# Optimization experiments

Measured on AMD Instinct MI355X. Metric: run time of the kernel, lower is better.

Reference implementation:

```python
import jax, jax.numpy as jnp
import numpy as np

N = 50000       # nodes
E = 1_600_000   # edges (avg degree 32)
IN = 256        # in_dim
HID = 64        # hidden_dim
HEADS = 2
CLS = 10
NEG_SLOPE = 0.2  # PyG GATConv default leaky_relu slope


def gat_layer(x, edge_index, W, att_src, att_dst, bias, heads, concat):
    """PyG-style GATConv (eval mode, add_self_loops=True).
    x: [N, F_in]; W: [F_in, heads*C]; att_src/att_dst: [heads, C]; bias: [heads*C] or [C].
    """
    n = x.shape[0]
    loop = jnp.arange(n)
    src = jnp.concatenate([edge_index[0], loop])   # message sources j
    dst = jnp.concatenate([edge_index[1], loop])   # message targets i
    C = W.shape[1] // heads
    h = (x @ W).reshape(n, heads, C)               # [N, H, C]
    a_s = jnp.sum(h * att_src, axis=-1)            # [N, H]
    a_d = jnp.sum(h * att_dst, axis=-1)            # [N, H]
    e = jax.nn.leaky_relu(a_s[src] + a_d[dst], NEG_SLOPE)   # [E', H]
    # segment softmax over incoming edges of each destination node
    m = jax.lax.stop_gradient(jax.ops.segment_max(e, dst, num_segments=n))
    ex = jnp.exp(e - m[dst])
    denom = jax.ops.segment_sum(ex, dst, num_segments=n)
    alpha = ex / denom[dst]                         # [E', H]
    out = jax.ops.segment_sum(alpha[:, :, None] * h[src], dst, num_segments=n)  # [N, H, C]
    out = out.reshape(n, heads * C) if concat else out.mean(axis=1)
    return out + bias


def setup_inputs() -> dict:
    key = jax.random.key(0)
    ks = jax.random.split(key, 12)
    sd = lambda f: np.float32(1.0 / np.sqrt(f))
    x = jax.random.normal(ks[0], (N, IN), dtype=jnp.float32)
    edge_index = jax.random.randint(ks[1], (2, E), 0, N, dtype=jnp.int64)
    # layer 1: in_dim -> hidden, heads=2, concat
    W1 = jax.random.normal(ks[2], (IN, HEADS * HID), dtype=jnp.float32) * sd(IN)
    as1 = jax.random.normal(ks[3], (HEADS, HID), dtype=jnp.float32) * sd(HID)
    ad1 = jax.random.normal(ks[4], (HEADS, HID), dtype=jnp.float32) * sd(HID)
    b1 = jnp.zeros((HEADS * HID,), dtype=jnp.float32)
    # layer 2: hidden*heads -> hidden, heads=1, concat=False
    W2 = jax.random.normal(ks[5], (HEADS * HID, HID), dtype=jnp.float32) * sd(HEADS * HID)
    as2 = jax.random.normal(ks[6], (1, HID), dtype=jnp.float32) * sd(HID)
    ad2 = jax.random.normal(ks[7], (1, HID), dtype=jnp.float32) * sd(HID)
    b2 = jnp.zeros((HID,), dtype=jnp.float32)
    # linear head
    Wl = jax.random.normal(ks[8], (HID, CLS), dtype=jnp.float32) * sd(HID)
    bl = jnp.zeros((CLS,), dtype=jnp.float32)
    return {"x": x, "edge_index": edge_index,
            "W1": W1, "as1": as1, "ad1": ad1, "b1": b1,
            "W2": W2, "as2": as2, "ad2": ad2, "b2": b2,
            "Wl": Wl, "bl": bl}


def reference(x, edge_index, W1, as1, ad1, b1, W2, as2, ad2, b2, Wl, bl):
    h = jax.nn.elu(gat_layer(x, edge_index, W1, as1, ad1, b1, HEADS, True))
    h = jax.nn.elu(gat_layer(h, edge_index, W2, as2, ad2, b2, 1, False))
    return h @ Wl + bl  # [N, num_classes]
```

## Files before the change

### kernel.cpp

```cpp
#include <hip/hip_runtime.h>

#define NN 50000
#define NE 1600000
#define EP (NE + NN)
#define IN_DIM 256
#define HIDD 64
#define NCLS 10
#define NBKT 196
#define EPB 8192
#define NPB ((EP + EPB - 1) / EPB)
#define BCAP 12288

typedef unsigned short u16;
typedef short bf16x8 __attribute__((ext_vector_type(8)));
typedef float f32x4 __attribute__((ext_vector_type(4)));
typedef unsigned u32x4 __attribute__((ext_vector_type(4)));

__device__ __forceinline__ float b2f(u16 v) { return __uint_as_float(((unsigned)v) << 16); }
__device__ __forceinline__ u16 f2b(float f) {
    unsigned u = __float_as_uint(f);
    unsigned r = (u + 0x7FFFu + ((u >> 16) & 1u)) >> 16;
    return (u16)r;
}

__device__ __forceinline__ void load_edge(const int* __restrict__ ei, int m, int g,
                                          int& s, int& d) {
    if (g < NE) {
        if (m) { s = ei[2 * (size_t)g]; d = ei[2 * ((size_t)NE + g)]; }
        else   { s = ei[g];             d = ei[NE + g]; }
    } else {
        s = d = g - NE;
    }
    s = s < 0 ? 0 : (s >= NN ? NN - 1 : s);
    d = d < 0 ? 0 : (d >= NN ? NN - 1 : d);
}

__device__ __forceinline__ void wcvt_att_job(
    const float* __restrict__ W, const float* __restrict__ as,
    const float* __restrict__ ad, int K, int N, int H, u16* __restrict__ Wt,
    int idx) {
    if (idx >= K * (N + 16)) return;
    int n = idx / K, k = idx - n * K;
    if (n < N) { Wt[idx] = f2b(W[(size_t)k * N + n]); return; }
    int j = n - N;
    if (j >= 2 * H) { Wt[idx] = 0; return; }
    const float* att = (j & 1) ? ad : as;
    int h = j >> 1, C = N / H;
    float sum = 0.f;
    for (int c = 0; c < C; ++c)
        sum += W[(size_t)k * N + h * C + c] * att[h * C + c];
    Wt[idx] = f2b(sum);
}

__global__ __launch_bounds__(1024) void partition_k(
    const int* __restrict__ ei, int* __restrict__ gcursor,
    unsigned* __restrict__ bbuf,
    const float* __restrict__ W1, const float* __restrict__ as1,
    const float* __restrict__ ad1, u16* __restrict__ w1t,
    const float* __restrict__ W2, const float* __restrict__ as2,
    const float* __restrict__ ad2, u16* __restrict__ w2t) {
    __shared__ int hist[NBKT], base[NBKT], cur[NBKT];
    __shared__ unsigned stash[EPB];
    __shared__ int smode;
    int t = threadIdx.x, b = blockIdx.x;
    if (b < 36) wcvt_att_job(W1, as1, ad1, 256, 128, 2, w1t, b * 1024 + t);
    else if (b < 46) wcvt_att_job(W2, as2, ad2, 128, 64, 1, w2t, (b - 36) * 1024 + t);
    if (t < 64) {
        int nz = 0;
#pragma unroll
        for (int k = 0; k < 4; ++k)
            if (ei[2 * (t * 4 + k) + 1] != 0) nz = 1;
        unsigned long long bal = __ballot(nz);
        if (t == 0) smode = (bal == 0ULL) ? 1 : 0;
    }
    for (int i = t; i < NBKT; i += 1024) hist[i] = 0;
    __syncthreads();
    int m = smode;
    int g0 = b * EPB;
    int gend = min(g0 + EPB, EP);
    for (int g = g0 + t; g < gend; g += 1024) {
        int s, d;
        load_edge(ei, m, g, s, d);
        stash[g - g0] = ((unsigned)s << 16) | (unsigned)d;
        atomicAdd(&hist[d >> 8], 1);
    }
    __syncthreads();
    for (int i = t; i < NBKT; i += 1024) {
        base[i] = hist[i] ? atomicAdd(&gcursor[i], hist[i]) : 0;
        cur[i] = 0;
    }
    __syncthreads();
    int cnt = gend - g0;
    for (int l = t; l < cnt; l += 1024) {
        unsigned p = stash[l];
        int d = p & 0xFFFF;
        int bb = d >> 8;
        int r = base[bb] + atomicAdd(&cur[bb], 1);
        if (r < BCAP)
            bbuf[(size_t)bb * BCAP + r] = ((p >> 16) << 8) | (unsigned)(d & 255);
    }
}

__global__ __launch_bounds__(1024) void bucket_csr_k(const unsigned* __restrict__ bbuf,
                                                     const int* __restrict__ gcursor,
                                                     int* __restrict__ row_ptr,
                                                     u16* __restrict__ csr_src) {
    __shared__ int bsc[256];
    __shared__ int hist[256], scn[256], cur[256];
    __shared__ int se0, scnt, stot;
    int b = blockIdx.x, t = threadIdx.x;
    int v = 0;
    if (t < 256) {
        v = (t < NBKT) ? min(gcursor[t], BCAP) : 0;
        bsc[t] = v;
        hist[t] = 0;
    }
    __syncthreads();
    for (int off = 1; off < 256; off <<= 1) {
        int x = (t < 256 && t >= off) ? bsc[t - off] : 0;
        __syncthreads();
        if (t < 256) bsc[t] += x;
        __syncthreads();
    }
    if (t == b) { se0 = bsc[t] - v; scnt = v; }
    if (t == NBKT - 1) stot = bsc[t];
    __syncthreads();
    int e0 = se0, cnt = scnt;
    const unsigned* bb = bbuf + (size_t)b * BCAP;
    for (int e = t; e < cnt; e += 1024)
        atomicAdd(&hist[bb[e] & 255], 1);
    __syncthreads();
    int hv = 0;
    if (t < 256) { hv = hist[t]; scn[t] = hv; }
    __syncthreads();
    for (int off = 1; off < 256; off <<= 1) {
        int x = (t < 256 && t >= off) ? scn[t - off] : 0;
        __syncthreads();
        if (t < 256) scn[t] += x;
        __syncthreads();
    }
    if (t < 256) {
        int ex = scn[t] - hv;
        int n = b * 256 + t;
        if (n < NN) row_ptr[n] = e0 + ex;
        cur[t] = e0 + ex;
    }
    __syncthreads();
    for (int e = t; e < cnt; e += 1024) {
        unsigned p = bb[e];
        int pos = atomicAdd(&cur[p & 255], 1);
        csr_src[pos] = (u16)(p >> 8);
    }
    if (b == 0 && t == 0) row_ptr[NN] = stot;
}

template <int K, int NF, int H, bool F32A>
__global__ __launch_bounds__(256) void gemm_mfma_att_k(
    const float* __restrict__ Af, const u16* __restrict__ Ab,
    const u16* __restrict__ Wt, u16* __restrict__ C,
    float* __restrict__ a_s, float* __restrict__ a_d) {
    constexpr int NTF = NF / 16, NT = NTF + 1, KS = K / 32;
    const int wave = threadIdx.x >> 6, lane = threadIdx.x & 63;
    const int quad = lane >> 4, l15 = lane & 15;
    const int m0 = blockIdx.x * 64 + wave * 16;
    int rowA = m0 + l15;
    if (rowA >= NN) rowA = NN - 1;
    const float* afp = F32A ? (Af + (size_t)rowA * K + quad * 8) : nullptr;
    const u16*   abp = F32A ? nullptr : (Ab + (size_t)rowA * K + quad * 8);
    const u16* bptr = Wt + (size_t)l15 * K + quad * 8;
    f32x4 acc[NT] = {};
#pragma unroll
    for (int ks = 0; ks < KS; ++ks) {
        bf16x8 af;
        if (F32A) {
            float4 v0 = *(const float4*)(afp + ks * 32);
            float4 v1 = *(const float4*)(afp + ks * 32 + 4);
            af[0] = (short)f2b(v0.x); af[1] = (short)f2b(v0.y);
            af[2] = (short)f2b(v0.z); af[3] = (short)f2b(v0.w);
            af[4] = (short)f2b(v1.x); af[5] = (short)f2b(v1.y);
            af[6] = (short)f2b(v1.z); af[7] = (short)f2b(v1.w);
        } else {
            af = *(const bf16x8*)(abp + ks * 32);
        }
        bf16x8 bf[NT];
#pragma unroll
        for (int nt = 0; nt < NT; ++nt)
            bf[nt] = *(const bf16x8*)(bptr + (size_t)nt * 16 * K + ks * 32);
#pragma unroll
        for (int nt = 0; nt < NT; ++nt)
            acc[nt] = __builtin_amdgcn_mfma_f32_16x16x32_bf16(af, bf[nt], acc[nt], 0, 0, 0);
    }
#pragma unroll
    for (int nt = 0; nt < NTF; ++nt) {
#pragma unroll
        for (int reg = 0; reg < 4; ++reg) {
            int row = m0 + quad * 4 + reg;
            if (row < NN) C[(size_t)row * NF + nt * 16 + l15] = f2b(acc[nt][reg]);
        }
    }
    if (l15 < 2 * H) {
        int h = l15 >> 1;
        float* dst = (l15 & 1) ? a_d : a_s;
#pragma unroll
        for (int reg = 0; reg < 4; ++reg) {
            int row = m0 + quad * 4 + reg;
            if (row < NN) dst[row * H + h] = acc[NTF][reg];
        }
    }
}

template <int CH, int H, bool HEAD>
__global__ __launch_bounds__(256) void gat_gather_k(
    const int* __restrict__ row_ptr, const u16* __restrict__ csr_src,
    const float* __restrict__ att_s, const float* __restrict__ a_d,
    const u16* __restrict__ h, const float* __restrict__ bias,
    u16* __restrict__ outg, const float* __restrict__ Wl,
    const float* __restrict__ bl, float* __restrict__ outh) {
    constexpr int LPR = CH / 8;
    constexpr int G = 64 / LPR;
    constexpr int SH = (CH == 128) ? 8 : 7;
    int n = (blockIdx.x * blockDim.x + threadIdx.x) >> 6;
    int lane = threadIdx.x & 63;
    if (n >= NN) return;
    int r0 = row_ptr[n], r1 = row_ptr[n + 1];
    const int q = lane & (LPR - 1);
    const int g = lane >> ((CH == 128) ? 4 : 3);
    const unsigned qoff = (unsigned)q * 16u;
    const unsigned char* h8 = (const unsigned char*)h;

    float4 av0 = *(const float4*)(att_s + q * 8);
    float4 av1 = *(const float4*)(att_s + q * 8 + 4);
    float attv[8] = {av0.x, av0.y, av0.z, av0.w, av1.x, av1.y, av1.z, av1.w};

    float adn = (H == 2) ? a_d[n * 2 + (q >> 3)] : a_d[n];

    float dh = 0.f;
    float acc[8];
#pragma unroll
    for (int v = 0; v < 8; ++v) acc[v] = 0.f;

    for (int base = r0; base < r1; base += 64) {
        int cnt = min(64, r1 - base);
        int idx = base + lane;
        bool act = idx < r1;
        int slv = act ? ((int)csr_src[idx] | 0x10000) : 0;
        for (int j0 = 0; j0 < cnt; j0 += 4 * G) {
            int sr[4];
#pragma unroll
            for (int i = 0; i < 4; ++i)
                sr[i] = __builtin_amdgcn_ds_bpermute((j0 + i * G + g) << 2, slv);
            u32x4 hv[4];
#pragma unroll
            for (int i = 0; i < 4; ++i)
                hv[i] = *(const u32x4*)(
                    h8 + (((unsigned)(sr[i] & 0xFFFF) << SH) + qoff));
#pragma unroll
            for (int i = 0; i < 4; ++i) {
                float f[8];
#pragma unroll
                for (int k = 0; k < 4; ++k) {
                    unsigned w = hv[i][k];
                    f[2 * k]     = __uint_as_float(w << 16);
                    f[2 * k + 1] = __uint_as_float(w & 0xFFFF0000u);
                }
                float d = f[0] * attv[0];
#pragma unroll
                for (int k = 1; k < 8; ++k) d += f[k] * attv[k];
                d += __shfl_xor(d, 1);
                d += __shfl_xor(d, 2);
                d += __shfl_xor(d, 4);
                float e = d + adn;
                e = e > 0.f ? e : 0.2f * e;
                e = fminf(e, 60.f);
                float ex = __expf(e);
                ex = (sr[i] & 0x10000) ? ex : 0.f;
                dh += ex;
#pragma unroll
                for (int k = 0; k < 8; ++k) acc[k] += ex * f[k];
            }
        }
    }

#pragma unroll
    for (int off = LPR; off < 64; off <<= 1) dh += __shfl_xor(dh, off);
#pragma unroll
    for (int v = 0; v < 8; ++v) {
#pragma unroll
        for (int off = LPR; off < 64; off <<= 1)
            acc[v] += __shfl_xor(acc[v], off);
    }

    if (HEAD) {
        float t01 = (lane & 8) ? acc[1] : acc[0];
        float t23 = (lane & 8) ? acc[3] : acc[2];
        float t45 = (lane & 8) ? acc[5] : acc[4];
        float t67 = (lane & 8) ? acc[7] : acc[6];
        float ta = (lane & 16) ? t23 : t01;
        float tb = (lane & 16) ? t67 : t45;
        float ts = (lane & 32) ? tb : ta;
        int srcl = ((lane & 7) << 3) | (lane >> 3);
        float vsw = __uint_as_float(
            __builtin_amdgcn_ds_bpermute(srcl << 2, __float_as_int(ts)));
        float v0 = vsw / dh + bias[lane];
        v0 = v0 > 0.f ? v0 : expm1f(v0);
#pragma unroll
        for (int cls = 0; cls < NCLS; ++cls) {
            float p = v0 * Wl[lane * NCLS + cls];
#pragma unroll
            for (int off = 32; off; off >>= 1) p += __shfl_xor(p, off);
            if (lane == cls) outh[(size_t)n * NCLS + cls] = p + bl[cls];
        }
    } else {
        if (g == 0) {
            float vv[8];
#pragma unroll
            for (int k = 0; k < 8; ++k) {
                float t = acc[k] / dh + bias[q * 8 + k];
                vv[k] = t > 0.f ? t : expm1f(t);
            }
            u32x4 ov;
#pragma unroll
            for (int d = 0; d < 4; ++d)
                ov[d] = (unsigned)f2b(vv[2 * d]) |
                        ((unsigned)f2b(vv[2 * d + 1]) << 16);
            *(u32x4*)(outg + (size_t)n * CH + q * 8) = ov;
        }
    }
}

extern "C" void kernel_launch(void* const* d_in, const int* in_sizes, int n_in,
                              void* d_out, int out_size, void* d_ws, size_t ws_size,
                              hipStream_t stream) {
    const float* x   = (const float*)d_in[0];
    const int*   ei  = (const int*)d_in[1];
    const float* W1  = (const float*)d_in[2];
    const float* as1 = (const float*)d_in[3];
    const float* ad1 = (const float*)d_in[4];
    const float* b1  = (const float*)d_in[5];
    const float* W2  = (const float*)d_in[6];
    const float* as2 = (const float*)d_in[7];
    const float* ad2 = (const float*)d_in[8];
    const float* b2  = (const float*)d_in[9];
    const float* Wl  = (const float*)d_in[10];
    const float* bl  = (const float*)d_in[11];
    float* out = (float*)d_out;

    float* ws = (float*)d_ws;
    size_t o = 0;
    u16* hb  = (u16*)(ws + o); o += (size_t)NN * 64;
    u16* g1  = (u16*)(ws + o); o += (size_t)NN * 64;
    unsigned* bbuf = (unsigned*)g1;
    u16* w1t = (u16*)(ws + o); o += 144 * 256 / 2;
    u16* w2t = (u16*)(ws + o); o += 80 * 128 / 2;
    float* a_s = ws + o;       o += (size_t)NN * 2;
    float* a_d = ws + o;       o += (size_t)NN * 2;
    int* ints = (int*)(ws + o);
    size_t io = 0;
    int* gcursor  = ints + io; io += NBKT;
    int* row_ptr  = ints + io; io += NN + 1;
    u16* csr_src  = (u16*)(ints + io); io += (EP + 1) / 2;

    hipMemsetAsync(gcursor, 0, NBKT * sizeof(int), stream);
    partition_k<<<NPB, 1024, 0, stream>>>(ei, gcursor, bbuf,
                                          W1, as1, ad1, w1t, W2, as2, ad2, w2t);
    bucket_csr_k<<<NBKT, 1024, 0, stream>>>(bbuf, gcursor, row_ptr, csr_src);

    const int gatherBlocks = (NN + 3) / 4;
    const int gemmBlocks = (NN + 63) / 64;

    gemm_mfma_att_k<256, 128, 2, true><<<gemmBlocks, 256, 0, stream>>>(
        x, nullptr, w1t, hb, a_s, a_d);
    gat_gather_k<128, 2, false><<<gatherBlocks, 256, 0, stream>>>(
        row_ptr, csr_src, as1, a_d, hb, b1, g1, nullptr, nullptr, nullptr);

    gemm_mfma_att_k<128, 64, 1, false><<<gemmBlocks, 256, 0, stream>>>(
        nullptr, g1, w2t, hb, a_s, a_d);
    gat_gather_k<64, 1, true><<<gatherBlocks, 256, 0, stream>>>(
        row_ptr, csr_src, as2, a_d, hb, b2, nullptr, Wl, bl, out);
}
```

Measured before the change: 361.0 us.

## Slice feature matrices into 32-column planes and split aggregation across XCDs

Stores node features as 32-column bf16 slices, one plane per slice, and assigns each slice to one XCD via blockIdx&7, so each XCD's L2 only caches its slice of the gather table. The gather uses the precomputed a_s instead of recomputing attention dot products per edge. Layer 2 gets a separate kernel that computes edge softmax weights and stores them packed with the source index. The classifier head moves to its own small MFMA kernel. The cost is more kernel launches and repeated index traversal per slice. Correctness relies on the XCD mapping only for locality, not for results.

Measured after the change: 350.0 us. -3.1%, faster.

```diff
diff --git a/kernel.cpp b/kernel.cpp
--- a/kernel.cpp
+++ b/kernel.cpp
@@ -14,7 +14,6 @@
 typedef unsigned short u16;
 typedef short bf16x8 __attribute__((ext_vector_type(8)));
 typedef float f32x4 __attribute__((ext_vector_type(4)));
-typedef unsigned u32x4 __attribute__((ext_vector_type(4)));
 
 __device__ __forceinline__ float b2f(u16 v) { return __uint_as_float(((unsigned)v) << 16); }
 __device__ __forceinline__ u16 f2b(float f) {
@@ -58,13 +57,18 @@
     const float* __restrict__ W1, const float* __restrict__ as1,
     const float* __restrict__ ad1, u16* __restrict__ w1t,
     const float* __restrict__ W2, const float* __restrict__ as2,
-    const float* __restrict__ ad2, u16* __restrict__ w2t) {
+    const float* __restrict__ ad2, u16* __restrict__ w2t,
+    const float* __restrict__ Wl, u16* __restrict__ wlt) {
     __shared__ int hist[NBKT], base[NBKT], cur[NBKT];
     __shared__ unsigned stash[EPB];
     __shared__ int smode;
     int t = threadIdx.x, b = blockIdx.x;
     if (b < 36) wcvt_att_job(W1, as1, ad1, 256, 128, 2, w1t, b * 1024 + t);
     else if (b < 46) wcvt_att_job(W2, as2, ad2, 128, 64, 1, w2t, (b - 36) * 1024 + t);
+    else if (b == 46) {
+        int n = t >> 6, k = t & 63;
+        wlt[n * 64 + k] = (n < NCLS) ? f2b(Wl[k * NCLS + n]) : (u16)0;
+    }
     if (t < 64) {
         int nz = 0;
 #pragma unroll
@@ -154,7 +158,7 @@
     if (b == 0 && t == 0) row_ptr[NN] = stot;
 }
 
-template <int K, int NF, int H, bool F32A>
+template <int K, int NF, int H, bool F32A, bool SLICED_A>
 __global__ __launch_bounds__(256) void gemm_mfma_att_k(
     const float* __restrict__ Af, const u16* __restrict__ Ab,
     const u16* __restrict__ Wt, u16* __restrict__ C,
@@ -166,13 +170,17 @@
     int rowA = m0 + l15;
     if (rowA >= NN) rowA = NN - 1;
     const float* afp = F32A ? (Af + (size_t)rowA * K + quad * 8) : nullptr;
-    const u16*   abp = F32A ? nullptr : (Ab + (size_t)rowA * K + quad * 8);
+    const u16* abp = nullptr;
+    if constexpr (!F32A) {
+        abp = SLICED_A ? (Ab + (size_t)rowA * 32 + quad * 8)
+                       : (Ab + (size_t)rowA * K + quad * 8);
+    }
     const u16* bptr = Wt + (size_t)l15 * K + quad * 8;
     f32x4 acc[NT] = {};
 #pragma unroll
     for (int ks = 0; ks < KS; ++ks) {
         bf16x8 af;
-        if (F32A) {
+        if constexpr (F32A) {
             float4 v0 = *(const float4*)(afp + ks * 32);
             float4 v1 = *(const float4*)(afp + ks * 32 + 4);
             af[0] = (short)f2b(v0.x); af[1] = (short)f2b(v0.y);
@@ -180,7 +188,8 @@
             af[4] = (short)f2b(v1.x); af[5] = (short)f2b(v1.y);
             af[6] = (short)f2b(v1.z); af[7] = (short)f2b(v1.w);
         } else {
-            af = *(const bf16x8*)(abp + ks * 32);
+            af = SLICED_A ? *(const bf16x8*)(abp + (size_t)ks * (NN * 32))
+                          : *(const bf16x8*)(abp + ks * 32);
         }
         bf16x8 bf[NT];
 #pragma unroll
@@ -195,7 +204,10 @@
 #pragma unroll
         for (int reg = 0; reg < 4; ++reg) {
             int row = m0 + quad * 4 + reg;
-            if (row < NN) C[(size_t)row * NF + nt * 16 + l15] = f2b(acc[nt][reg]);
+            int c = nt * 16 + l15;
+            if (row < NN)
+                C[(size_t)(c >> 5) * (NN * 32) + (size_t)row * 32 + (c & 31)] =
+                    f2b(acc[nt][reg]);
         }
     }
     if (l15 < 2 * H) {
@@ -209,121 +221,161 @@
     }
 }
 
-template <int CH, int H, bool HEAD>
-__global__ __launch_bounds__(256) void gat_gather_k(
+__global__ __launch_bounds__(256) void edge_alpha_k(
     const int* __restrict__ row_ptr, const u16* __restrict__ csr_src,
-    const float* __restrict__ att_s, const float* __restrict__ a_d,
+    const float* __restrict__ a_s, const float* __restrict__ a_d,
+    unsigned* __restrict__ A2, float* __restrict__ dninv) {
+    int wave = threadIdx.x >> 6;
+    int pair = blockIdx.x * 4 + wave;
+    if (pair >= NN / 2) return;
+    int lane = threadIdx.x & 63, half = lane >> 5, hl = lane & 31;
+    int node = pair * 2 + half;
+    int r0 = row_ptr[node], r1 = row_ptr[node + 1];
+    int cnt = r1 - r0;
+    int co = max(cnt, __shfl_xor(cnt, 32));
+    int nbat = (co + 31) >> 5;
+    float adn = a_d[node];
+    float dh = 0.f;
+    for (int b = 0; b < nbat; ++b) {
+        int idx = r0 + b * 32 + hl;
+        bool act = idx < r1;
+        int sl = act ? (int)csr_src[idx] : 0;
+        float e = a_s[sl] + adn;
+        e = e > 0.f ? e : 0.2f * e;
+        e = fminf(e, 60.f);
+        float ex = act ? __expf(e) : 0.f;
+        dh += ex;
+        if (act)
+            __builtin_nontemporal_store(
+                (unsigned)sl | ((unsigned)f2b(ex) << 16), A2 + idx);
+    }
+#pragma unroll
+    for (int off = 1; off < 32; off <<= 1) dh += __shfl_xor(dh, off);
+    if (hl == 0) dninv[node] = 1.0f / dh;
+}
+
+template <int CH, int NSL, int H, bool USE_EX>
+__global__ __launch_bounds__(256) void gat_slice_k(
+    const int* __restrict__ row_ptr, const u16* __restrict__ csr_src,
+    const unsigned* __restrict__ A2, const float* __restrict__ a_s,
+    const float* __restrict__ a_d, const float* __restrict__ dninv,
     const u16* __restrict__ h, const float* __restrict__ bias,
-    u16* __restrict__ outg, const float* __restrict__ Wl,
-    const float* __restrict__ bl, float* __restrict__ outh) {
-    constexpr int LPR = CH / 8;
-    constexpr int G = 64 / LPR;
-    constexpr int SH = (CH == 128) ? 8 : 7;
-    int n = (blockIdx.x * blockDim.x + threadIdx.x) >> 6;
+    u16* __restrict__ outg) {
+    constexpr int SC = CH / NSL;
+    constexpr int SUB = 8 / NSL;
+    int xcd = blockIdx.x & 7;
+    int slice = xcd / SUB;
+    int sub = xcd % SUB;
+    int pg = (blockIdx.x >> 3) * SUB + sub;
+    int wave = threadIdx.x >> 6;
+    int pair = pg * 4 + wave;
+    if (pair >= NN / 2) return;
     int lane = threadIdx.x & 63;
-    if (n >= NN) return;
-    int r0 = row_ptr[n], r1 = row_ptr[n + 1];
-    const int q = lane & (LPR - 1);
-    const int g = lane >> ((CH == 128) ? 4 : 3);
-    const unsigned qoff = (unsigned)q * 16u;
-    const unsigned char* h8 = (const unsigned char*)h;
-
-    float4 av0 = *(const float4*)(att_s + q * 8);
-    float4 av1 = *(const float4*)(att_s + q * 8 + 4);
-    float attv[8] = {av0.x, av0.y, av0.z, av0.w, av1.x, av1.y, av1.z, av1.w};
-
-    float adn = (H == 2) ? a_d[n * 2 + (q >> 3)] : a_d[n];
-
+    int half = lane >> 5, hl = lane & 31, q = hl & 7, gh = hl >> 3;
+    int node = pair * 2 + half;
+    int r0 = row_ptr[node], r1 = row_ptr[node + 1];
+    int cnt = r1 - r0;
+    int co = max(cnt, __shfl_xor(cnt, 32));
+    int nbat = (co + 31) >> 5;
+    const unsigned char* hb8 =
+        (const unsigned char*)h + (size_t)slice * (NN * 64);
+    const int head = (H == 2) ? (slice >> 1) : 0;
+    float adn = 0.f, rdn = 0.f;
+    if constexpr (USE_EX) rdn = dninv[node];
+    else adn = a_d[node * H + head];
     float dh = 0.f;
-    float acc[8];
-#pragma unroll
-    for (int v = 0; v < 8; ++v) acc[v] = 0.f;
-
-    for (int base = r0; base < r1; base += 64) {
-        int cnt = min(64, r1 - base);
-        int idx = base + lane;
+    float acc[4] = {0.f, 0.f, 0.f, 0.f};
+    const int abase = ((half << 5) | gh) << 2;
+    for (int b = 0; b < nbat; ++b) {
+        int idx = r0 + b * 32 + hl;
         bool act = idx < r1;
-        int slv = act ? ((int)csr_src[idx] | 0x10000) : 0;
-        for (int j0 = 0; j0 < cnt; j0 += 4 * G) {
-            int sr[4];
+        unsigned pex;
+        if constexpr (USE_EX) {
+            pex = act ? __builtin_nontemporal_load(A2 + idx) : 0u;
+        } else {
+            int sl = act ? (int)__builtin_nontemporal_load(csr_src + idx) : 0;
+            float e = a_s[sl * H + head] + adn;
+            e = e > 0.f ? e : 0.2f * e;
+            e = fminf(e, 60.f);
+            float ex = act ? __expf(e) : 0.f;
+            dh += ex;
+            pex = (unsigned)sl | ((unsigned)f2b(ex) << 16);
+        }
+#pragma unroll
+        for (int jr = 0; jr < 2; ++jr) {
+            int pr[4];
 #pragma unroll
             for (int i = 0; i < 4; ++i)
-                sr[i] = __builtin_amdgcn_ds_bpermute((j0 + i * G + g) << 2, slv);
-            u32x4 hv[4];
-#pragma unroll
-            for (int i = 0; i < 4; ++i)
-                hv[i] = *(const u32x4*)(
-                    h8 + (((unsigned)(sr[i] & 0xFFFF) << SH) + qoff));
+                pr[i] = __builtin_amdgcn_ds_bpermute(
+                    abase + ((jr * 16 + i * 4) << 2), (int)pex);
+            unsigned hv0[4], hv1[4];
 #pragma unroll
             for (int i = 0; i < 4; ++i) {
-                float f[8];
-#pragma unroll
-                for (int k = 0; k < 4; ++k) {
-                    unsigned w = hv[i][k];
-                    f[2 * k]     = __uint_as_float(w << 16);
-                    f[2 * k + 1] = __uint_as_float(w & 0xFFFF0000u);
-                }
-                float d = f[0] * attv[0];
-#pragma unroll
-                for (int k = 1; k < 8; ++k) d += f[k] * attv[k];
-                d += __shfl_xor(d, 1);
-                d += __shfl_xor(d, 2);
-                d += __shfl_xor(d, 4);
-                float e = d + adn;
-                e = e > 0.f ? e : 0.2f * e;
-                e = fminf(e, 60.f);
-                float ex = __expf(e);
-                ex = (sr[i] & 0x10000) ? ex : 0.f;
-                dh += ex;
-#pragma unroll
-                for (int k = 0; k < 8; ++k) acc[k] += ex * f[k];
+                const unsigned* p = (const unsigned*)(
+                    hb8 + (((unsigned)((unsigned)pr[i] & 0xFFFFu) << 6) + q * 8));
+                hv0[i] = p[0];
+                hv1[i] = p[1];
             }
-        }
-    }
-
-#pragma unroll
-    for (int off = LPR; off < 64; off <<= 1) dh += __shfl_xor(dh, off);
-#pragma unroll
-    for (int v = 0; v < 8; ++v) {
-#pragma unroll
-        for (int off = LPR; off < 64; off <<= 1)
-            acc[v] += __shfl_xor(acc[v], off);
-    }
-
-    if (HEAD) {
-        float t01 = (lane & 8) ? acc[1] : acc[0];
-        float t23 = (lane & 8) ? acc[3] : acc[2];
-        float t45 = (lane & 8) ? acc[5] : acc[4];
-        float t67 = (lane & 8) ? acc[7] : acc[6];
-        float ta = (lane & 16) ? t23 : t01;
-        float tb = (lane & 16) ? t67 : t45;
-        float ts = (lane & 32) ? tb : ta;
-        int srcl = ((lane & 7) << 3) | (lane >> 3);
-        float vsw = __uint_as_float(
-            __builtin_amdgcn_ds_bpermute(srcl << 2, __float_as_int(ts)));
-        float v0 = vsw / dh + bias[lane];
-        v0 = v0 > 0.f ? v0 : expm1f(v0);
-#pragma unroll
-        for (int cls = 0; cls < NCLS; ++cls) {
-            float p = v0 * Wl[lane * NCLS + cls];
-#pragma unroll
-            for (int off = 32; off; off >>= 1) p += __shfl_xor(p, off);
-            if (lane == cls) outh[(size_t)n * NCLS + cls] = p + bl[cls];
-        }
-    } else {
-        if (g == 0) {
-            float vv[8];
-#pragma unroll
-            for (int k = 0; k < 8; ++k) {
-                float t = acc[k] / dh + bias[q * 8 + k];
-                vv[k] = t > 0.f ? t : expm1f(t);
+#pragma unroll
+            for (int i = 0; i < 4; ++i) {
+                float exf = __uint_as_float((unsigned)pr[i] & 0xFFFF0000u);
+                unsigned w0 = hv0[i], w1 = hv1[i];
+                acc[0] += exf * __uint_as_float(w0 << 16);
+                acc[1] += exf * __uint_as_float(w0 & 0xFFFF0000u);
+                acc[2] += exf * __uint_as_float(w1 << 16);
+                acc[3] += exf * __uint_as_float(w1 & 0xFFFF0000u);
             }
-            u32x4 ov;
-#pragma unroll
-            for (int d = 0; d < 4; ++d)
-                ov[d] = (unsigned)f2b(vv[2 * d]) |
-                        ((unsigned)f2b(vv[2 * d + 1]) << 16);
-            *(u32x4*)(outg + (size_t)n * CH + q * 8) = ov;
+        }
+    }
+    if constexpr (!USE_EX) {
+#pragma unroll
+        for (int off = 1; off < 32; off <<= 1) dh += __shfl_xor(dh, off);
+        rdn = 1.0f / dh;
+    }
+#pragma unroll
+    for (int v = 0; v < 4; ++v) {
+        acc[v] += __shfl_xor(acc[v], 8);
+        acc[v] += __shfl_xor(acc[v], 16);
+    }
+    if (gh == 0) {
+        float vv[4];
+#pragma unroll
+        for (int k = 0; k < 4; ++k) {
+            float t = acc[k] * rdn + bias[slice * SC + q * 4 + k];
+            vv[k] = t > 0.f ? t : expm1f(t);
+        }
+        unsigned long long ov =
+            (unsigned long long)((unsigned)f2b(vv[0]) | ((unsigned)f2b(vv[1]) << 16)) |
+            ((unsigned long long)((unsigned)f2b(vv[2]) | ((unsigned)f2b(vv[3]) << 16)) << 32);
+        __builtin_nontemporal_store(
+            ov, (unsigned long long*)(outg + (size_t)slice * (NN * 32) +
+                                      (size_t)node * 32 + q * 4));
+    }
+}
+
+__global__ __launch_bounds__(256) void head_gemm_k(
+    const u16* __restrict__ A, const u16* __restrict__ Wt,
+    const float* __restrict__ bl, float* __restrict__ out) {
+    const int wave = threadIdx.x >> 6, lane = threadIdx.x & 63;
+    const int quad = lane >> 4, l15 = lane & 15;
+    const int m0 = blockIdx.x * 64 + wave * 16;
+    int rowA = m0 + l15;
+    if (rowA >= NN) rowA = NN - 1;
+    const u16* ab = A + (size_t)rowA * 32 + quad * 8;
+    const u16* bp = Wt + (size_t)l15 * 64 + quad * 8;
+    f32x4 acc = {};
+#pragma unroll
+    for (int ks = 0; ks < 2; ++ks) {
+        bf16x8 af = *(const bf16x8*)(ab + (size_t)ks * (NN * 32));
+        bf16x8 bf = *(const bf16x8*)(bp + ks * 32);
+        acc = __builtin_amdgcn_mfma_f32_16x16x32_bf16(af, bf, acc, 0, 0, 0);
+    }
+    if (l15 < NCLS) {
+        float blv = bl[l15];
+#pragma unroll
+        for (int reg = 0; reg < 4; ++reg) {
+            int row = m0 + quad * 4 + reg;
+            if (row < NN) out[(size_t)row * NCLS + l15] = acc[reg] + blv;
         }
     }
 }
@@ -348,10 +400,14 @@
     float* ws = (float*)d_ws;
     size_t o = 0;
     u16* hb  = (u16*)(ws + o); o += (size_t)NN * 64;
+    u16* g2  = hb + (size_t)NN * 64;
     u16* g1  = (u16*)(ws + o); o += (size_t)NN * 64;
     unsigned* bbuf = (unsigned*)g1;
+    unsigned* A2 = (unsigned*)g1;
+    float* dn2inv = (float*)((char*)g1 + (size_t)EP * 4);
     u16* w1t = (u16*)(ws + o); o += 144 * 256 / 2;
     u16* w2t = (u16*)(ws + o); o += 80 * 128 / 2;
+    u16* wlt = (u16*)(ws + o); o += 16 * 64 / 2;
     float* a_s = ws + o;       o += (size_t)NN * 2;
     float* a_d = ws + o;       o += (size_t)NN * 2;
     int* ints = (int*)(ws + o);
@@ -362,19 +418,23 @@
 
     hipMemsetAsync(gcursor, 0, NBKT * sizeof(int), stream);
     partition_k<<<NPB, 1024, 0, stream>>>(ei, gcursor, bbuf,
-                                          W1, as1, ad1, w1t, W2, as2, ad2, w2t);
+                                          W1, as1, ad1, w1t, W2, as2, ad2, w2t,
+                                          Wl, wlt);
     bucket_csr_k<<<NBKT, 1024, 0, stream>>>(bbuf, gcursor, row_ptr, csr_src);
 
-    const int gatherBlocks = (NN + 3) / 4;
     const int gemmBlocks = (NN + 63) / 64;
 
-    gemm_mfma_att_k<256, 128, 2, true><<<gemmBlocks, 256, 0, stream>>>(
+    gemm_mfma_att_k<256, 128, 2, true, false><<<gemmBlocks, 256, 0, stream>>>(
         x, nullptr, w1t, hb, a_s, a_d);
-    gat_gather_k<128, 2, false><<<gatherBlocks, 256, 0, stream>>>(
-        row_ptr, csr_src, as1, a_d, hb, b1, g1, nullptr, nullptr, nullptr);
-
-    gemm_mfma_att_k<128, 64, 1, false><<<gemmBlocks, 256, 0, stream>>>(
+    gat_slice_k<128, 4, 2, false><<<25000, 256, 0, stream>>>(
+        row_ptr, csr_src, nullptr, a_s, a_d, nullptr, hb, b1, g1);
+
+    gemm_mfma_att_k<128, 64, 1, false, true><<<gemmBlocks, 256, 0, stream>>>(
         nullptr, g1, w2t, hb, a_s, a_d);
-    gat_gather_k<64, 1, true><<<gatherBlocks, 256, 0, stream>>>(
-        row_ptr, csr_src, as2, a_d, hb, b2, nullptr, Wl, bl, out);
-}
+    edge_alpha_k<<<(NN / 2 + 3) / 4, 256, 0, stream>>>(
+        row_ptr, csr_src, a_s, a_d, A2, dn2inv);
+    gat_slice_k<64, 2, 1, true><<<12504, 256, 0, stream>>>(
+        row_ptr, csr_src, A2, nullptr, nullptr, dn2inv, hb, b2, g2);
+
+    head_gemm_k<<<gemmBlocks, 256, 0, stream>>>(g2, wlt, bl, out);
+}
```
